# Kernel tuning notes

Measured on AMD Instinct MI355X. Metric: run time of the kernel, lower is better.

## Reference

```python
import jax, jax.numpy as jnp
import numpy as np

B, T, C, H = 512, 256, 128, 128


def setup_inputs() -> dict:
    key = jax.random.key(0)
    kx, kk, kq, kv = jax.random.split(key, 4)
    x = jax.random.normal(kx, (B, T, C), dtype=jnp.float32)
    # weights stored as [in, out]; Linear(bias=False) is x @ W
    Wk = jax.random.normal(kk, (C, H), dtype=jnp.float32) * 0.02
    Wq = jax.random.normal(kq, (C, H), dtype=jnp.float32) * 0.02
    Wv = jax.random.normal(kv, (C, H), dtype=jnp.float32) * 0.02
    return {"x": x, "Wk": Wk, "Wq": Wq, "Wv": Wv}


def reference(x, Wk, Wq, Wv):
    Bx, Tx, Cx = x.shape
    k = jnp.einsum("btc,ch->bth", x, Wk)
    q = jnp.einsum("btc,ch->bth", x, Wq)
    v = jnp.einsum("btc,ch->bth", x, Wv)
    scale = Cx ** -0.5  # NOTE: original scales by n_embd (C), not head_size
    wei = jnp.einsum("bth,bsh->bts", q, k) * scale  # [B, T, T]
    causal = jnp.tril(jnp.ones((Tx, Tx), dtype=bool))
    wei = jnp.where(causal[None, :, :], wei, -jnp.inf)
    wei = jax.nn.softmax(wei, axis=-1)
    # dropout is identity in eval mode
    out = jnp.einsum("bts,bsh->bth", wei, v)  # [B, T, H]
    return (out, k, v)  # matches (out, present=(k, v))
```

## Files before the change

kernel.cpp:

```cpp
#include <hip/hip_runtime.h>

typedef unsigned short u16;
typedef __attribute__((ext_vector_type(8))) short short8;
typedef __attribute__((ext_vector_type(4))) float float4v;

#define BTH (512*256*128)
#define MASKV (-30000.0f)

__device__ __forceinline__ u16 f2bf(float f){
    union{float f; unsigned i;} v; v.f = f;
    unsigned x = v.i;
    unsigned r = (x + 0x7FFFu + ((x >> 16) & 1u)) >> 16;
    return (u16)r;
}

__global__ void wt_kernel(const float* __restrict__ Wq, const float* __restrict__ Wk,
                          const float* __restrict__ Wv, u16* __restrict__ WT){
    int idx = blockIdx.x * 256 + threadIdx.x;
    int w   = idx >> 14;
    int rem = idx & 16383;
    int n = rem >> 7;
    int k = rem & 127;
    const float* src = (w == 0) ? Wq : (w == 1) ? Wk : Wv;
    float val = src[k * 128 + n];
    if (w == 0) val *= 0.08838834764831845f;
    WT[idx] = f2bf(val);
}

__global__ __launch_bounds__(512, 2) void fused_kernel(const float* __restrict__ x,
                                                       const u16* __restrict__ WT,
                                                       float* __restrict__ dout){
    __shared__ u16 Kbuf [4 * 256 * 32];
    __shared__ u16 VTbuf[8 * 128 * 32];

    int b = blockIdx.x;
    int tid = threadIdx.x;
    int w = tid >> 6, lane = tid & 63, lq = lane & 15, quad = lane >> 4;

    const float* xb   = x    + (size_t)b * 256 * 128;
    float*       oout = dout + (size_t)b * 256 * 128;
    float*       kout = dout + (size_t)BTH     + (size_t)b * 256 * 128;
    float*       vout = dout + (size_t)2 * BTH + (size_t)b * 256 * 128;

    const int rtg[2] = { w, w + 8 };

    short8 ax[2][4];
    #pragma unroll
    for (int rt = 0; rt < 2; rt++){
        #pragma unroll
        for (int ks = 0; ks < 4; ks++){
            const float* px = xb + (size_t)(rtg[rt]*16 + lq)*128 + ks*32 + quad*8;
            float4v lo = *(const float4v*)px;
            float4v hi = *(const float4v*)(px + 4);
            short8 s;
            #pragma unroll
            for (int j = 0; j < 4; j++){
                s[j]     = (short)f2bf(lo[j]);
                s[j + 4] = (short)f2bf(hi[j]);
            }
            ax[rt][ks] = s;
        }
    }

    u16* qs = Kbuf + w * 4096;
    short8 qf[2][4];
    #pragma unroll
    for (int rt = 0; rt < 2; rt++){
        #pragma unroll
        for (int ht = 0; ht < 8; ht++){
            short8 bw[4];
            #pragma unroll
            for (int ks = 0; ks < 4; ks++)
                bw[ks] = *(const short8*)(WT + (size_t)(ht*16 + lq)*128 + ks*32 + quad*8);
            float4v c = {0.f,0.f,0.f,0.f};
            #pragma unroll
            for (int ks = 0; ks < 4; ks++)
                c = __builtin_amdgcn_mfma_f32_16x16x32_bf16(ax[rt][ks], bw[ks], c, 0, 0, 0);
            #pragma unroll
            for (int r = 0; r < 4; r++)
                qs[(quad*4 + r)*136 + ht*16 + lq] = f2bf(c[r]);
        }
        #pragma unroll
        for (int ks = 0; ks < 4; ks++)
            qf[rt][ks] = *(const short8*)(qs + lq*136 + ks*32 + quad*8);
    }
    __syncthreads();

    #pragma unroll
    for (int rt = 0; rt < 2; rt++){
        #pragma unroll
        for (int ht = 0; ht < 8; ht++){
            short8 bw[4];
            #pragma unroll
            for (int ks = 0; ks < 4; ks++)
                bw[ks] = *(const short8*)(WT + (size_t)16384 + (size_t)(ht*16 + lq)*128 + ks*32 + quad*8);
            float4v c = {0.f,0.f,0.f,0.f};
            #pragma unroll
            for (int ks = 0; ks < 4; ks++)
                c = __builtin_amdgcn_mfma_f32_16x16x32_bf16(ax[rt][ks], bw[ks], c, 0, 0, 0);
            #pragma unroll
            for (int r = 0; r < 4; r++){
                int key = rtg[rt]*16 + quad*4 + r;
                kout[(size_t)key*128 + ht*16 + lq] = c[r];
                Kbuf[(ht>>1)*8192 + key*32 + (ht&1)*16 + lq] = f2bf(c[r]);
            }
        }
    }

    #pragma unroll
    for (int ht = 0; ht < 8; ht++){
        short8 bv[4];
        #pragma unroll
        for (int ks = 0; ks < 4; ks++)
            bv[ks] = *(const short8*)(WT + (size_t)2*16384 + (size_t)(ht*16 + lq)*128 + ks*32 + quad*8);
        #pragma unroll
        for (int rt = 0; rt < 2; rt++){
            float4v c = {0.f,0.f,0.f,0.f};
            #pragma unroll
            for (int ks = 0; ks < 4; ks++)
                c = __builtin_amdgcn_mfma_f32_16x16x32_bf16(ax[rt][ks], bv[ks], c, 0, 0, 0);
            #pragma unroll
            for (int r = 0; r < 4; r++)
                vout[(size_t)(rtg[rt]*16 + quad*4 + r)*128 + ht*16 + lq] = c[r];
            float4v ct = {0.f,0.f,0.f,0.f};
            #pragma unroll
            for (int ks = 0; ks < 4; ks++)
                ct = __builtin_amdgcn_mfma_f32_16x16x32_bf16(bv[ks], ax[rt][ks], ct, 0, 0, 0);
            int t = rtg[rt]*16 + lq;
            int e0 = (t>>5)*4096 + (t&31);
            #pragma unroll
            for (int r = 0; r < 4; r++)
                VTbuf[e0 + (ht*16 + quad*4 + r)*32] = f2bf(ct[r]);
        }
    }
    __syncthreads();

    float4v s[2][16];
    float lsum[2][4];
    #pragma unroll
    for (int rt = 0; rt < 2; rt++){
        int rg = rtg[rt];
        #pragma unroll
        for (int kt = 0; kt < 16; kt++){
            if (kt <= rg){
                float4v c = {0.f,0.f,0.f,0.f};
                #pragma unroll
                for (int ks = 0; ks < 4; ks++){
                    short8 bb = *(const short8*)(Kbuf + ks*8192 + (kt*16 + lq)*32 + quad*8);
                    c = __builtin_amdgcn_mfma_f32_16x16x32_bf16(qf[rt][ks], bb, c, 0, 0, 0);
                }
                if (kt == rg){
                    #pragma unroll
                    for (int r = 0; r < 4; r++)
                        if (kt*16 + lq > rg*16 + quad*4 + r) c[r] = MASKV;
                }
                s[rt][kt] = c;
            }
        }
        #pragma unroll
        for (int r = 0; r < 4; r++){
            float mx = MASKV;
            #pragma unroll
            for (int kt = 0; kt < 16; kt++)
                if (kt <= rg) mx = fmaxf(mx, s[rt][kt][r]);
            mx = fmaxf(mx, __shfl_xor(mx, 1));
            mx = fmaxf(mx, __shfl_xor(mx, 2));
            mx = fmaxf(mx, __shfl_xor(mx, 4));
            mx = fmaxf(mx, __shfl_xor(mx, 8));
            float rs = 0.f;
            #pragma unroll
            for (int kt = 0; kt < 16; kt++)
                if (kt <= rg){
                    float pv = __expf(s[rt][kt][r] - mx);
                    s[rt][kt][r] = pv;
                    rs += pv;
                }
            rs += __shfl_xor(rs, 1);
            rs += __shfl_xor(rs, 2);
            rs += __shfl_xor(rs, 4);
            rs += __shfl_xor(rs, 8);
            lsum[rt][r] = rs;
        }
    }
    __syncthreads();

    float4v oacc[2][8];
    #pragma unroll
    for (int rt = 0; rt < 2; rt++)
        #pragma unroll
        for (int o = 0; o < 8; o++) oacc[rt][o] = (float4v){0.f,0.f,0.f,0.f};

    u16* psw = Kbuf + w * 4096;
    #pragma unroll
    for (int kb = 0; kb < 4; kb++){
        #pragma unroll
        for (int rt = 0; rt < 2; rt++){
            int rg = rtg[rt];
            if (kb <= (rg >> 2)){
                #pragma unroll
                for (int kt2 = 0; kt2 < 4; kt2++){
                    int kt = kb*4 + kt2;
                    #pragma unroll
                    for (int r = 0; r < 4; r++){
                        float pv = (kt <= rg) ? s[rt][kt][r] : 0.f;
                        psw[rt*1152 + (quad*4 + r)*72 + kt2*16 + lq] = f2bf(pv);
                    }
                }
            }
        }
        #pragma unroll
        for (int rt = 0; rt < 2; rt++){
            if (kb <= (rtg[rt] >> 2)){
                #pragma unroll
                for (int k2 = 0; k2 < 2; k2++){
                    short8 pa = *(const short8*)(psw + rt*1152 + lq*72 + k2*32 + quad*8);
                    #pragma unroll
                    for (int o = 0; o < 8; o++){
                        short8 vb = *(const short8*)(VTbuf + (kb*2 + k2)*4096 + (o*16 + lq)*32 + quad*8);
                        oacc[rt][o] = __builtin_amdgcn_mfma_f32_16x16x32_bf16(pa, vb, oacc[rt][o], 0, 0, 0);
                    }
                }
            }
        }
    }

    #pragma unroll
    for (int rt = 0; rt < 2; rt++){
        #pragma unroll
        for (int r = 0; r < 4; r++){
            float inv = 1.0f / lsum[rt][r];
            int row = rtg[rt]*16 + quad*4 + r;
            #pragma unroll
            for (int o = 0; o < 8; o++)
                oout[(size_t)row*128 + o*16 + lq] = oacc[rt][o][r] * inv;
        }
    }
}

extern "C" void kernel_launch(void* const* d_in, const int* in_sizes, int n_in,
                              void* d_out, int out_size, void* d_ws, size_t ws_size,
                              hipStream_t stream){
    const float* x  = (const float*)d_in[0];
    const float* Wk = (const float*)d_in[1];
    const float* Wq = (const float*)d_in[2];
    const float* Wv = (const float*)d_in[3];
    float* out = (float*)d_out;
    u16* WT = (u16*)d_ws;

    wt_kernel   <<<192, 256, 0, stream>>>(Wq, Wk, Wv, WT);
    fused_kernel<<<512, 512, 0, stream>>>(x, WT, out);
}
```

Measured before the change: 354.2 us.

## Switch to online softmax over key blocks to cut register pressure

The kernel no longer holds the full row of attention scores for two row tiles in registers. It processes keys in blocks of 64 with a running max and running sum, rescaling the output accumulators per block, and writes probabilities to a new dedicated LDS staging buffer. This removes one __syncthreads and shrinks the live score state. The launch bound is relaxed from 2 to 1 blocks per CU, which the larger LDS footprint already forced, so the compiler can use more VGPRs. The cost is extra exp and rescale work per block, clamping of scores, and more shared memory.

```diff
diff --git a/kernel.cpp b/kernel.cpp
--- a/kernel.cpp
+++ b/kernel.cpp
@@ -27,11 +27,12 @@
     WT[idx] = f2bf(val);
 }
 
-__global__ __launch_bounds__(512, 2) void fused_kernel(const float* __restrict__ x,
+__global__ __launch_bounds__(512, 1) void fused_kernel(const float* __restrict__ x,
                                                        const u16* __restrict__ WT,
                                                        float* __restrict__ dout){
     __shared__ u16 Kbuf [4 * 256 * 32];
     __shared__ u16 VTbuf[8 * 128 * 32];
+    __shared__ u16 ps   [8 * 1152];
 
     int b = blockIdx.x;
     int tid = threadIdx.x;
@@ -62,7 +63,7 @@
         }
     }
 
-    u16* qs = Kbuf + w * 4096;
+    u16* qs = VTbuf + w * 4096;
     short8 qf[2][4];
     #pragma unroll
     for (int rt = 0; rt < 2; rt++){
@@ -135,100 +136,96 @@
     }
     __syncthreads();
 
-    float4v s[2][16];
-    float lsum[2][4];
-    #pragma unroll
-    for (int rt = 0; rt < 2; rt++){
-        int rg = rtg[rt];
-        #pragma unroll
-        for (int kt = 0; kt < 16; kt++){
-            if (kt <= rg){
-                float4v c = {0.f,0.f,0.f,0.f};
-                #pragma unroll
-                for (int ks = 0; ks < 4; ks++){
-                    short8 bb = *(const short8*)(Kbuf + ks*8192 + (kt*16 + lq)*32 + quad*8);
-                    c = __builtin_amdgcn_mfma_f32_16x16x32_bf16(qf[rt][ks], bb, c, 0, 0, 0);
-                }
-                if (kt == rg){
+    float4v oacc[2][8];
+    float mrun[2][4], lrun[2][4];
+    #pragma unroll
+    for (int rt = 0; rt < 2; rt++){
+        #pragma unroll
+        for (int o = 0; o < 8; o++) oacc[rt][o] = (float4v){0.f,0.f,0.f,0.f};
+        #pragma unroll
+        for (int r = 0; r < 4; r++){ mrun[rt][r] = MASKV; lrun[rt][r] = 0.f; }
+    }
+    u16* psw = ps + w * 1152;
+
+    #pragma unroll
+    for (int kb = 0; kb < 4; kb++){
+        #pragma unroll
+        for (int rt = 0; rt < 2; rt++){
+            int rg = rtg[rt];
+            if (kb*4 > rg) continue;
+
+            float4v s4[4];
+            #pragma unroll
+            for (int kt2 = 0; kt2 < 4; kt2++){
+                int kt = kb*4 + kt2;
+                float4v c = {MASKV, MASKV, MASKV, MASKV};
+                if (kt <= rg){
+                    c = (float4v){0.f,0.f,0.f,0.f};
+                    #pragma unroll
+                    for (int ks = 0; ks < 4; ks++){
+                        short8 bb = *(const short8*)(Kbuf + ks*8192 + (kt*16 + lq)*32 + quad*8);
+                        c = __builtin_amdgcn_mfma_f32_16x16x32_bf16(qf[rt][ks], bb, c, 0, 0, 0);
+                    }
                     #pragma unroll
                     for (int r = 0; r < 4; r++)
-                        if (kt*16 + lq > rg*16 + quad*4 + r) c[r] = MASKV;
+                        c[r] = fminf(fmaxf(c[r], MASKV), 30000.0f);
+                    if (kt == rg){
+                        #pragma unroll
+                        for (int r = 0; r < 4; r++)
+                            if (kt*16 + lq > rg*16 + quad*4 + r) c[r] = MASKV;
+                    }
                 }
-                s[rt][kt] = c;
-            }
-        }
-        #pragma unroll
-        for (int r = 0; r < 4; r++){
-            float mx = MASKV;
-            #pragma unroll
-            for (int kt = 0; kt < 16; kt++)
-                if (kt <= rg) mx = fmaxf(mx, s[rt][kt][r]);
-            mx = fmaxf(mx, __shfl_xor(mx, 1));
-            mx = fmaxf(mx, __shfl_xor(mx, 2));
-            mx = fmaxf(mx, __shfl_xor(mx, 4));
-            mx = fmaxf(mx, __shfl_xor(mx, 8));
-            float rs = 0.f;
-            #pragma unroll
-            for (int kt = 0; kt < 16; kt++)
-                if (kt <= rg){
-                    float pv = __expf(s[rt][kt][r] - mx);
-                    s[rt][kt][r] = pv;
+                s4[kt2] = c;
+            }
+            #pragma unroll
+            for (int r = 0; r < 4; r++){
+                float mx = fmaxf(fmaxf(s4[0][r], s4[1][r]), fmaxf(s4[2][r], s4[3][r]));
+                mx = fmaxf(mx, __shfl_xor(mx, 1));
+                mx = fmaxf(mx, __shfl_xor(mx, 2));
+                mx = fmaxf(mx, __shfl_xor(mx, 4));
+                mx = fmaxf(mx, __shfl_xor(mx, 8));
+                float mnew = fmaxf(mrun[rt][r], mx);
+                float alpha = __expf(mrun[rt][r] - mnew);
+                float rs = 0.f;
+                #pragma unroll
+                for (int kt2 = 0; kt2 < 4; kt2++){
+                    float pv = __expf(s4[kt2][r] - mnew);
+                    s4[kt2][r] = pv;
                     rs += pv;
                 }
-            rs += __shfl_xor(rs, 1);
-            rs += __shfl_xor(rs, 2);
-            rs += __shfl_xor(rs, 4);
-            rs += __shfl_xor(rs, 8);
-            lsum[rt][r] = rs;
-        }
-    }
-    __syncthreads();
-
-    float4v oacc[2][8];
-    #pragma unroll
-    for (int rt = 0; rt < 2; rt++)
-        #pragma unroll
-        for (int o = 0; o < 8; o++) oacc[rt][o] = (float4v){0.f,0.f,0.f,0.f};
-
-    u16* psw = Kbuf + w * 4096;
-    #pragma unroll
-    for (int kb = 0; kb < 4; kb++){
-        #pragma unroll
-        for (int rt = 0; rt < 2; rt++){
-            int rg = rtg[rt];
-            if (kb <= (rg >> 2)){
-                #pragma unroll
-                for (int kt2 = 0; kt2 < 4; kt2++){
-                    int kt = kb*4 + kt2;
-                    #pragma unroll
-                    for (int r = 0; r < 4; r++){
-                        float pv = (kt <= rg) ? s[rt][kt][r] : 0.f;
-                        psw[rt*1152 + (quad*4 + r)*72 + kt2*16 + lq] = f2bf(pv);
-                    }
+                rs += __shfl_xor(rs, 1);
+                rs += __shfl_xor(rs, 2);
+                rs += __shfl_xor(rs, 4);
+                rs += __shfl_xor(rs, 8);
+                lrun[rt][r] = lrun[rt][r] * alpha + rs;
+                mrun[rt][r] = mnew;
+                #pragma unroll
+                for (int o = 0; o < 8; o++) oacc[rt][o][r] *= alpha;
+            }
+            #pragma unroll
+            for (int kt2 = 0; kt2 < 4; kt2++)
+                #pragma unroll
+                for (int r = 0; r < 4; r++)
+                    psw[(quad*4 + r)*72 + kt2*16 + lq] = f2bf(s4[kt2][r]);
+            short8 pa0 = *(const short8*)(psw + lq*72 + quad*8);
+            short8 pa1 = *(const short8*)(psw + lq*72 + 32 + quad*8);
+            #pragma unroll
+            for (int k2 = 0; k2 < 2; k2++){
+                short8 pa = (k2 == 0) ? pa0 : pa1;
+                #pragma unroll
+                for (int o = 0; o < 8; o++){
+                    short8 vb = *(const short8*)(VTbuf + (kb*2 + k2)*4096 + (o*16 + lq)*32 + quad*8);
+                    oacc[rt][o] = __builtin_amdgcn_mfma_f32_16x16x32_bf16(pa, vb, oacc[rt][o], 0, 0, 0);
                 }
             }
         }
-        #pragma unroll
-        for (int rt = 0; rt < 2; rt++){
-            if (kb <= (rtg[rt] >> 2)){
-                #pragma unroll
-                for (int k2 = 0; k2 < 2; k2++){
-                    short8 pa = *(const short8*)(psw + rt*1152 + lq*72 + k2*32 + quad*8);
-                    #pragma unroll
-                    for (int o = 0; o < 8; o++){
-                        short8 vb = *(const short8*)(VTbuf + (kb*2 + k2)*4096 + (o*16 + lq)*32 + quad*8);
-                        oacc[rt][o] = __builtin_amdgcn_mfma_f32_16x16x32_bf16(pa, vb, oacc[rt][o], 0, 0, 0);
-                    }
-                }
-            }
-        }
     }
 
     #pragma unroll
     for (int rt = 0; rt < 2; rt++){
         #pragma unroll
         for (int r = 0; r < 4; r++){
-            float inv = 1.0f / lsum[rt][r];
+            float inv = 1.0f / lrun[rt][r];
             int row = rtg[rt]*16 + quad*4 + r;
             #pragma unroll
             for (int o = 0; o < 8; o++)
```

New measurement: 324.3 us. -8.4%, faster.
